# Kernel tuning notes

Measured on AMD Instinct MI355X. Metric: run time of the kernel, lower is better.

The kernel has to match this reference:

```python
import jax, jax.numpy as jnp
import numpy as np

NUM_GROUPS = 32
EPS = 1e-05
HT_MIN = -1.0
HT_MAX = 1.0


def setup_inputs() -> dict:
    key = jax.random.key(0)
    k1, k2, k3 = jax.random.split(key, 3)
    B, IN, OUT = 4096, 2048, 2048
    x = jax.random.normal(k1, (B, IN), dtype=jnp.float32)
    # kaiming-uniform-ish scale for weight, uniform bias bound 1/sqrt(in)
    weight = jax.random.normal(k2, (OUT, IN), dtype=jnp.float32) * (1.0 / np.sqrt(IN))
    bias = jax.random.uniform(k3, (OUT,), dtype=jnp.float32, minval=-1.0 / np.sqrt(IN), maxval=1.0 / np.sqrt(IN))
    gn_weight = jnp.ones((OUT,), dtype=jnp.float32)
    gn_bias = jnp.zeros((OUT,), dtype=jnp.float32)
    return {"x": x, "weight": weight, "bias": bias, "gn_weight": gn_weight, "gn_bias": gn_bias}


def reference(x, weight, bias, gn_weight, gn_bias):
    # Linear: y = x @ W^T + b   -> [B, OUT]
    y = jnp.einsum("bi,oi->bo", x, weight) + bias
    B, C = y.shape
    G = NUM_GROUPS
    yg = y.reshape(B, G, C // G)
    mean = jnp.mean(yg, axis=-1, keepdims=True)
    var = jnp.mean(jnp.square(yg), axis=-1, keepdims=True) - jnp.square(mean)
    yn = ((yg - mean) * jax.lax.rsqrt(var + EPS)).reshape(B, C)
    out = yn * gn_weight + gn_bias
    return jnp.clip(out, HT_MIN, HT_MAX)
```

## Files before the change

### kernel.cpp

```cpp
#include <hip/hip_runtime.h>
#include <stdint.h>

#define B_ROWS 4096
#define C_OUT  2048
#define C_IN   2048
#define EPS    1e-5f

typedef __attribute__((ext_vector_type(8))) short bf16x8;
typedef __attribute__((ext_vector_type(4))) float f32x4;

__device__ __forceinline__ unsigned short f2bf(float f) {
    uint32_t u = __float_as_uint(f);
    uint32_t r = (u + 0x7fffu + ((u >> 16) & 1u)) >> 16;
    return (unsigned short)r;
}

__global__ void cvt_f32_bf16_kernel(const float* __restrict__ x,
                                    const float* __restrict__ w,
                                    unsigned short* __restrict__ xb,
                                    unsigned short* __restrict__ wb,
                                    int nx4, int nw4) {
    int i = blockIdx.x * blockDim.x + threadIdx.x;
    const float* src;
    unsigned short* dst;
    if (i < nx4) {
        src = x; dst = xb;
    } else {
        i -= nx4;
        if (i >= nw4) return;
        src = w; dst = wb;
    }
    float4 v = ((const float4*)src)[i];
    ushort4 o;
    o.x = f2bf(v.x); o.y = f2bf(v.y); o.z = f2bf(v.z); o.w = f2bf(v.w);
    ((ushort4*)dst)[i] = o;
}

__global__ __launch_bounds__(512, 2)
void gemm_gn_kernel(const unsigned short* __restrict__ A,
                    const unsigned short* __restrict__ W,
                    const float* __restrict__ bias,
                    const float* __restrict__ gnw,
                    const float* __restrict__ gnb,
                    float* __restrict__ out) {
    __shared__ __align__(16) unsigned short smem[3 * 24576];

    const int bc   = blockIdx.x;
    const int br   = blockIdx.y;
    const int tid  = threadIdx.x;
    const int lane = tid & 63;
    const int wave = tid >> 6;
    const int wr   = wave >> 1;
    const int wc   = wave & 1;
    const int c16  = lane & 15;
    const int quad = lane >> 4;

    f32x4 acc[4][4];
#pragma unroll
    for (int i = 0; i < 4; i++)
#pragma unroll
        for (int j = 0; j < 4; j++) acc[i][j] = (f32x4){0.f, 0.f, 0.f, 0.f};

    const int r0 = tid >> 3;
    const int qo = ((tid & 7) ^ (r0 & 7)) * 8;
    const unsigned short* gA = A + (size_t)(br * 256 + r0) * C_IN + qo;
    const unsigned short* gB = W + (size_t)(bc * 128 + r0) * C_IN + qo;
    const int t8 = tid * 8;

#define STAGE_H(dst, k0, half)                                                                      \
    do {                                                                                            \
        _Pragma("unroll")                                                                           \
        for (int n = (half) * 2; n < (half) * 2 + 2; n++)                                           \
            __builtin_amdgcn_global_load_lds(                                                       \
                (const __attribute__((address_space(1))) void*)(gA + (size_t)(n * 64) * C_IN + (k0)), \
                (__attribute__((address_space(3))) void*)((dst) + n * 4096 + t8), 16, 0, 0);        \
        __builtin_amdgcn_global_load_lds(                                                           \
            (const __attribute__((address_space(1))) void*)(gB + (size_t)((half) * 64) * C_IN + (k0)), \
            (__attribute__((address_space(3))) void*)((dst) + 16384 + (half) * 4096 + t8), 16, 0, 0); \
    } while (0)

    unsigned short* bf0 = smem;
    unsigned short* bf1 = smem + 24576;
    unsigned short* bf2 = smem + 49152;

    STAGE_H(bf0, 0, 0);  STAGE_H(bf0, 0, 1);
    STAGE_H(bf1, 64, 0); STAGE_H(bf1, 64, 1);
    asm volatile("s_waitcnt vmcnt(6)" ::: "memory");
    __builtin_amdgcn_s_barrier();

    const unsigned short* pr = bf0;
    const unsigned short* pn = bf1;
    unsigned short*       ps = bf2;

#pragma unroll 1
    for (int kt = 0; kt < 32; ++kt) {
        const int k2 = (kt + 2) * 64;
        bf16x8 a[4], bq[4];

        {
            const int qs = (quad ^ (c16 & 7)) * 8;
#pragma unroll
            for (int i = 0; i < 4; i++)
                a[i] = *(const bf16x8*)(pr + (wr * 64 + i * 16 + c16) * 64 + qs);
#pragma unroll
            for (int j = 0; j < 4; j++)
                bq[j] = *(const bf16x8*)(pr + 16384 + (wc * 64 + j * 16 + c16) * 64 + qs);
        }
        if (kt < 30) STAGE_H(ps, k2, 0);
        __builtin_amdgcn_s_barrier();
        asm volatile("s_waitcnt lgkmcnt(0)" ::: "memory");
        __builtin_amdgcn_sched_barrier(0);
        __builtin_amdgcn_s_setprio(1);
#pragma unroll
        for (int i = 0; i < 4; i++)
#pragma unroll
            for (int j = 0; j < 4; j++)
                acc[i][j] = __builtin_amdgcn_mfma_f32_16x16x32_bf16(a[i], bq[j], acc[i][j], 0, 0, 0);
        __builtin_amdgcn_s_setprio(0);
        __builtin_amdgcn_s_barrier();

        {
            const int qs = ((4 + quad) ^ (c16 & 7)) * 8;
#pragma unroll
            for (int i = 0; i < 4; i++)
                a[i] = *(const bf16x8*)(pr + (wr * 64 + i * 16 + c16) * 64 + qs);
#pragma unroll
            for (int j = 0; j < 4; j++)
                bq[j] = *(const bf16x8*)(pr + 16384 + (wc * 64 + j * 16 + c16) * 64 + qs);
        }
        if (kt < 30) STAGE_H(ps, k2, 1);
        __builtin_amdgcn_s_barrier();
        asm volatile("s_waitcnt lgkmcnt(0)" ::: "memory");
        __builtin_amdgcn_sched_barrier(0);
        __builtin_amdgcn_s_setprio(1);
#pragma unroll
        for (int i = 0; i < 4; i++)
#pragma unroll
            for (int j = 0; j < 4; j++)
                acc[i][j] = __builtin_amdgcn_mfma_f32_16x16x32_bf16(a[i], bq[j], acc[i][j], 0, 0, 0);
        __builtin_amdgcn_s_setprio(0);

        if (kt < 30)       asm volatile("s_waitcnt vmcnt(6)" ::: "memory");
        else if (kt == 30) asm volatile("s_waitcnt vmcnt(0)" ::: "memory");
        __builtin_amdgcn_s_barrier();

        const unsigned short* tmp = pr;
        pr = pn;
        pn = ps;
        ps = (unsigned short*)tmp;
    }

    const int colbase = bc * 128 + wc * 64;
    const int rowbase = br * 256 + wr * 64;
    float bv[4], gw[4], gb[4];
#pragma unroll
    for (int j = 0; j < 4; j++) {
        int col = colbase + j * 16 + c16;
        bv[j] = bias[col];
        gw[j] = gnw[col];
        gb[j] = gnb[col];
    }
#pragma unroll
    for (int i = 0; i < 4; i++) {
#pragma unroll
        for (int r = 0; r < 4; r++) {
            float s = 0.f, ss = 0.f;
#pragma unroll
            for (int j = 0; j < 4; j++) {
                float v = acc[i][j][r] + bv[j];
                acc[i][j][r] = v;
                s += v;
                ss += v * v;
            }
#pragma unroll
            for (int m = 1; m < 16; m <<= 1) {
                s  += __shfl_xor(s, m, 64);
                ss += __shfl_xor(ss, m, 64);
            }
            float mean = s * (1.f / 64.f);
            float var  = ss * (1.f / 64.f) - mean * mean;
            float rstd = rsqrtf(var + EPS);
            int row = rowbase + i * 16 + quad * 4 + r;
            float* orow = out + (size_t)row * C_OUT;
#pragma unroll
            for (int j = 0; j < 4; j++) {
                float v = (acc[i][j][r] - mean) * rstd * gw[j] + gb[j];
                v = fminf(1.f, fmaxf(-1.f, v));
                orow[colbase + j * 16 + c16] = v;
            }
        }
    }
}

extern "C" void kernel_launch(void* const* d_in, const int* in_sizes, int n_in,
                              void* d_out, int out_size, void* d_ws, size_t ws_size,
                              hipStream_t stream) {
    const float* x    = (const float*)d_in[0];
    const float* w    = (const float*)d_in[1];
    const float* bias = (const float*)d_in[2];
    const float* gnw  = (const float*)d_in[3];
    const float* gnb  = (const float*)d_in[4];
    float* out = (float*)d_out;

    unsigned short* xb = (unsigned short*)d_ws;
    unsigned short* wb = xb + (size_t)B_ROWS * C_IN;

    const int nx4 = B_ROWS * C_IN / 4;
    const int nw4 = C_OUT * C_IN / 4;
    cvt_f32_bf16_kernel<<<(nx4 + nw4 + 255) / 256, 256, 0, stream>>>(x, w, xb, wb, nx4, nw4);

    dim3 grid(C_OUT / 128, B_ROWS / 256);
    gemm_gn_kernel<<<grid, 512, 0, stream>>>(xb, wb, bias, gnw, gnb, out);
}
```

Measured before the change: 140.2 us.

## Double-buffer LDS fragment registers to overlap reads with MFMA and drop barriers

Keeps two sets of A/B register fragments so the second k-half is read from LDS while the first half's MFMAs run, and the next tile's first half is prefetched while the second half computes. Uses partial lgkmcnt waits instead of full drains and cuts the per-iteration barrier count from four to two. It also hoists the LDS offset computation out of the loop. The cost is higher VGPR pressure under launch_bounds(512,2), more intricate vmcnt/lgkmcnt accounting that risks races, and a possible occupancy drop.

```diff
diff --git a/kernel.cpp b/kernel.cpp
--- a/kernel.cpp
+++ b/kernel.cpp
@@ -83,6 +83,14 @@
     unsigned short* bf1 = smem + 24576;
     unsigned short* bf2 = smem + 49152;
 
+    const int qs0 = (quad ^ (c16 & 7)) * 8;
+    const int qs1 = ((4 + quad) ^ (c16 & 7)) * 8;
+    int offA[4], offB[4];
+#pragma unroll
+    for (int i = 0; i < 4; i++) offA[i] = (wr * 64 + i * 16 + c16) * 64;
+#pragma unroll
+    for (int j = 0; j < 4; j++) offB[j] = 16384 + (wc * 64 + j * 16 + c16) * 64;
+
     STAGE_H(bf0, 0, 0);  STAGE_H(bf0, 0, 1);
     STAGE_H(bf1, 64, 0); STAGE_H(bf1, 64, 1);
     asm volatile("s_waitcnt vmcnt(6)" ::: "memory");
@@ -92,57 +100,53 @@
     const unsigned short* pn = bf1;
     unsigned short*       ps = bf2;
 
+    bf16x8 a0[4], b0[4], a1[4], b1[4];
+#pragma unroll
+    for (int i = 0; i < 4; i++) a0[i] = *(const bf16x8*)(pr + offA[i] + qs0);
+#pragma unroll
+    for (int j = 0; j < 4; j++) b0[j] = *(const bf16x8*)(pr + offB[j] + qs0);
+
 #pragma unroll 1
     for (int kt = 0; kt < 32; ++kt) {
         const int k2 = (kt + 2) * 64;
-        bf16x8 a[4], bq[4];
-
-        {
-            const int qs = (quad ^ (c16 & 7)) * 8;
-#pragma unroll
-            for (int i = 0; i < 4; i++)
-                a[i] = *(const bf16x8*)(pr + (wr * 64 + i * 16 + c16) * 64 + qs);
-#pragma unroll
-            for (int j = 0; j < 4; j++)
-                bq[j] = *(const bf16x8*)(pr + 16384 + (wc * 64 + j * 16 + c16) * 64 + qs);
-        }
+
+#pragma unroll
+        for (int i = 0; i < 4; i++) a1[i] = *(const bf16x8*)(pr + offA[i] + qs1);
+#pragma unroll
+        for (int j = 0; j < 4; j++) b1[j] = *(const bf16x8*)(pr + offB[j] + qs1);
         if (kt < 30) STAGE_H(ps, k2, 0);
-        __builtin_amdgcn_s_barrier();
-        asm volatile("s_waitcnt lgkmcnt(0)" ::: "memory");
+        asm volatile("s_waitcnt lgkmcnt(8)" ::: "memory");
         __builtin_amdgcn_sched_barrier(0);
         __builtin_amdgcn_s_setprio(1);
 #pragma unroll
         for (int i = 0; i < 4; i++)
 #pragma unroll
             for (int j = 0; j < 4; j++)
-                acc[i][j] = __builtin_amdgcn_mfma_f32_16x16x32_bf16(a[i], bq[j], acc[i][j], 0, 0, 0);
+                acc[i][j] = __builtin_amdgcn_mfma_f32_16x16x32_bf16(a0[i], b0[j], acc[i][j], 0, 0, 0);
         __builtin_amdgcn_s_setprio(0);
-        __builtin_amdgcn_s_barrier();
-
-        {
-            const int qs = ((4 + quad) ^ (c16 & 7)) * 8;
-#pragma unroll
-            for (int i = 0; i < 4; i++)
-                a[i] = *(const bf16x8*)(pr + (wr * 64 + i * 16 + c16) * 64 + qs);
-#pragma unroll
-            for (int j = 0; j < 4; j++)
-                bq[j] = *(const bf16x8*)(pr + 16384 + (wc * 64 + j * 16 + c16) * 64 + qs);
+
+        if (kt < 30)       asm volatile("s_waitcnt vmcnt(3)" ::: "memory");
+        else if (kt == 30) asm volatile("s_waitcnt vmcnt(0)" ::: "memory");
+        if (kt < 31) {
+            __builtin_amdgcn_s_barrier();
+#pragma unroll
+            for (int i = 0; i < 4; i++) a0[i] = *(const bf16x8*)(pn + offA[i] + qs0);
+#pragma unroll
+            for (int j = 0; j < 4; j++) b0[j] = *(const bf16x8*)(pn + offB[j] + qs0);
+            if (kt < 30) STAGE_H(ps, k2, 1);
+            asm volatile("s_waitcnt lgkmcnt(8)" ::: "memory");
+        } else {
+            asm volatile("s_waitcnt lgkmcnt(0)" ::: "memory");
         }
-        if (kt < 30) STAGE_H(ps, k2, 1);
-        __builtin_amdgcn_s_barrier();
-        asm volatile("s_waitcnt lgkmcnt(0)" ::: "memory");
         __builtin_amdgcn_sched_barrier(0);
         __builtin_amdgcn_s_setprio(1);
 #pragma unroll
         for (int i = 0; i < 4; i++)
 #pragma unroll
             for (int j = 0; j < 4; j++)
-                acc[i][j] = __builtin_amdgcn_mfma_f32_16x16x32_bf16(a[i], bq[j], acc[i][j], 0, 0, 0);
+                acc[i][j] = __builtin_amdgcn_mfma_f32_16x16x32_bf16(a1[i], b1[j], acc[i][j], 0, 0, 0);
         __builtin_amdgcn_s_setprio(0);
-
-        if (kt < 30)       asm volatile("s_waitcnt vmcnt(6)" ::: "memory");
-        else if (kt == 30) asm volatile("s_waitcnt vmcnt(0)" ::: "memory");
-        __builtin_amdgcn_s_barrier();
+        if (kt < 31) __builtin_amdgcn_s_barrier();
 
         const unsigned short* tmp = pr;
         pr = pn;
```

After: 136.9 us. 1.02x faster.
